# Kernel optimization log

Measured on AMD Instinct MI355X. Metric: run time of the kernel, lower is better.

The kernel has to match this reference:

```python
import jax, jax.numpy as jnp
import numpy as np

B, T, D, H = 2, 2048, 1024, 16
DK = D // H  # 64


def setup_inputs() -> dict:
    key = jax.random.key(0)
    ks = jax.random.split(key, 13)
    s = 1.0 / np.sqrt(D)
    return {
        "x": jax.random.normal(ks[0], (B, T, D), jnp.float32),
        "Wq_w": jax.random.normal(ks[1], (D, D), jnp.float32) * s,
        "Wq_b": jax.random.normal(ks[2], (D,), jnp.float32) * 0.01,
        "Wk_w": jax.random.normal(ks[3], (D, D), jnp.float32) * s,
        "Wk_b": jax.random.normal(ks[4], (D,), jnp.float32) * 0.01,
        "Wv_w": jax.random.normal(ks[5], (D, D), jnp.float32) * s,
        "Wv_b": jax.random.normal(ks[6], (D,), jnp.float32) * 0.01,
        "Wo_w": jax.random.normal(ks[7], (D, D), jnp.float32) * s,
        "Wo_b": jax.random.normal(ks[8], (D,), jnp.float32) * 0.01,
        "qr": jax.random.normal(ks[9], (B, H, T, DK), jnp.float32),
        "qi": jax.random.normal(ks[10], (B, H, T, DK), jnp.float32),
        "kr": jax.random.normal(ks[11], (B, H, T, DK), jnp.float32),
        "ki": jax.random.normal(ks[12], (B, H, T, DK), jnp.float32),
    }


def _heads(y):
    # [B,T,D] -> [B,H,T,DK]
    return y.reshape(B, T, H, DK).transpose(0, 2, 1, 3)


def reference(x, Wq_w, Wq_b, Wk_w, Wk_b, Wv_w, Wv_b, Wo_w, Wo_b, qr, qi, kr, ki):
    Q = _heads(x @ Wq_w.T + Wq_b)
    K = _heads(x @ Wk_w.T + Wk_b)
    V = _heads(x @ Wv_w.T + Wv_b)
    # quantum noise: sin(atan2(imag, real))
    Q = Q + jnp.sin(jnp.arctan2(qi, qr))
    K = K + jnp.sin(jnp.arctan2(ki, kr))
    # Recursive fractal attention collapses: branches are identical and
    # deterministic, so (A1+A2)/2 == depth-0 attention at every level.
    scores = jnp.einsum("bhtd,bhsd->bhts", Q, K) / np.sqrt(DK).astype(np.float32)
    weights = jax.nn.softmax(scores, axis=-1)
    attn = jnp.einsum("bhts,bhsd->bhtd", weights, V)  # [B,H,T,DK]
    out = attn.transpose(0, 2, 1, 3).reshape(B, T, D)
    return out @ Wo_w.T + Wo_b
```

## Files before the change

kernel.cpp:

```cpp
#include <hip/hip_runtime.h>
#include <hip/hip_fp16.h>
#include <stdint.h>

typedef _Float16 half_t;
typedef _Float16 hf2 __attribute__((ext_vector_type(2)));
typedef _Float16 hf4 __attribute__((ext_vector_type(4)));
typedef _Float16 hf8 __attribute__((ext_vector_type(8)));
typedef float f32x16 __attribute__((ext_vector_type(16)));
typedef unsigned uint2_t __attribute__((ext_vector_type(2)));

#define LOG2E 1.4426950408889634f

__device__ __forceinline__ void gload16(const void* g, void* l) {
  __builtin_amdgcn_global_load_lds(
      (const __attribute__((address_space(1))) unsigned int*)g,
      (__attribute__((address_space(3))) unsigned int*)l, 16, 0, 0);
}

__device__ __forceinline__ unsigned packrtz(float a, float b) {
  auto h = __builtin_amdgcn_cvt_pkrtz(a, b);
  union { decltype(h) h2; unsigned u; } c;
  c.h2 = h;
  return c.u;
}

__device__ __forceinline__ float exp2fast(float x) {
#if __has_builtin(__builtin_amdgcn_exp2f)
  return __builtin_amdgcn_exp2f(x);
#else
  return exp2f(x);
#endif
}

__device__ __forceinline__ float psum2(unsigned pw, hf2 ones, float acc) {
#if __has_builtin(__builtin_amdgcn_fdot2)
  union { unsigned u; hf2 h; } c;
  c.u = pw;
  return __builtin_amdgcn_fdot2(c.h, ones, acc, false);
#else
  union { unsigned u; hf2 h; } c;
  c.u = pw;
  return acc + (float)c.h[0] + (float)c.h[1];
#endif
}

__global__ __launch_bounds__(256) void cvt_kernel(
    const float* __restrict__ x, const float* __restrict__ wq,
    const float* __restrict__ wk, const float* __restrict__ wv,
    const float* __restrict__ wo, half_t* __restrict__ xh,
    half_t* __restrict__ wh) {
  long e = ((long)blockIdx.x * 256 + threadIdx.x) * 16;
  const float* src;
  half_t* dst;
  if (e < 4194304L) {
    src = x + e;
    dst = xh + e;
  } else {
    long j = e - 4194304L;
    int w = (int)(j >> 20);
    long off = j & 1048575L;
    src = (w == 0 ? wq : w == 1 ? wk : w == 2 ? wv : wo) + off;
    dst = wh + ((long)w << 20) + off;
  }
  const float4* s4 = (const float4*)src;
  float4 f0 = s4[0], f1 = s4[1], f2 = s4[2], f3 = s4[3];
  hf8 o0 = {(half_t)f0.x, (half_t)f0.y, (half_t)f0.z, (half_t)f0.w,
            (half_t)f1.x, (half_t)f1.y, (half_t)f1.z, (half_t)f1.w};
  hf8 o1 = {(half_t)f2.x, (half_t)f2.y, (half_t)f2.z, (half_t)f2.w,
            (half_t)f3.x, (half_t)f3.y, (half_t)f3.z, (half_t)f3.w};
  *(hf8*)dst = o0;
  *(hf8*)(dst + 8) = o1;
}

template <int CUR>
__device__ __forceinline__ void gstep(bool stage, const half_t* __restrict__ A,
                                      const half_t* __restrict__ Bt,
                                      char* ldsb, int wid, int& goA, int& goB,
                                      int aof0, int aof1, int aof2, int aof3,
                                      int bof0, int bof1, int bof2, int bof3,
                                      f32x16 acc[2][2]) {
  if (stage) {
#pragma unroll
    for (int i = 0; i < 4; i++) {
      gload16(A + goA + i * 32768,
              ldsb + (CUR ^ 1) * 16384 + i * 4096 + wid * 1024);
      gload16(Bt + goB + i * 32768,
              ldsb + 32768 + (CUR ^ 1) * 16384 + i * 4096 + wid * 1024);
    }
    goA += 64;
    goB += 64;
  }
#pragma unroll
  for (int kc = 0; kc < 4; kc++) {
    const int ao = (kc == 0 ? aof0 : kc == 1 ? aof1 : kc == 2 ? aof2 : aof3);
    const int bo = (kc == 0 ? bof0 : kc == 1 ? bof1 : kc == 2 ? bof2 : bof3);
    hf8 af0 = *(const hf8*)(ldsb + CUR * 16384 + ao);
    hf8 af1 = *(const hf8*)(ldsb + CUR * 16384 + ao + 4096);
    hf8 bf0 = *(const hf8*)(ldsb + 32768 + CUR * 16384 + bo);
    hf8 bf1 = *(const hf8*)(ldsb + 32768 + CUR * 16384 + bo + 4096);
    acc[0][0] =
        __builtin_amdgcn_mfma_f32_32x32x16_f16(af0, bf0, acc[0][0], 0, 0, 0);
    acc[0][1] =
        __builtin_amdgcn_mfma_f32_32x32x16_f16(af0, bf1, acc[0][1], 0, 0, 0);
    acc[1][0] =
        __builtin_amdgcn_mfma_f32_32x32x16_f16(af1, bf0, acc[1][0], 0, 0, 0);
    acc[1][1] =
        __builtin_amdgcn_mfma_f32_32x32x16_f16(af1, bf1, acc[1][1], 0, 0, 0);
  }
  __syncthreads();
}

__device__ __forceinline__ void gemm_core(const half_t* __restrict__ A,
                                          const half_t* __restrict__ Bt,
                                          int m0, int n0, char* ldsb,
                                          f32x16 acc[2][2]) {
  const int tid = threadIdx.x;
  const int wid = tid >> 6;
  const int lane = tid & 63;
  const int l31 = lane & 31;
  const int hh = lane >> 5;
  const int wm = wid >> 1, wn = wid & 1;

#pragma unroll
  for (int mt = 0; mt < 2; mt++)
#pragma unroll
    for (int nt = 0; nt < 2; nt++)
#pragma unroll
      for (int i = 0; i < 16; i++) acc[mt][nt][i] = 0.f;

  const int rowb = tid >> 3;
  const int c16 = (tid & 7) ^ (rowb & 7);
  int goA = (m0 + rowb) * 1024 + c16 * 8;
  int goB = (n0 + rowb) * 1024 + c16 * 8;

  const int swz0 = (hh * 16) ^ ((l31 & 7) << 4);
  const int swz1 = (32 + hh * 16) ^ ((l31 & 7) << 4);
  const int swz2 = (64 + hh * 16) ^ ((l31 & 7) << 4);
  const int swz3 = (96 + hh * 16) ^ ((l31 & 7) << 4);
  const int arow = (wm * 64 + l31) * 128;
  const int brow = (wn * 64 + l31) * 128;
  const int aof0 = arow + swz0, aof1 = arow + swz1, aof2 = arow + swz2,
            aof3 = arow + swz3;
  const int bof0 = brow + swz0, bof1 = brow + swz1, bof2 = brow + swz2,
            bof3 = brow + swz3;

#pragma unroll
  for (int i = 0; i < 4; i++) {
    gload16(A + goA + i * 32768, ldsb + i * 4096 + wid * 1024);
    gload16(Bt + goB + i * 32768, ldsb + 32768 + i * 4096 + wid * 1024);
  }
  goA += 64;
  goB += 64;
  __syncthreads();

  for (int kp = 0; kp < 8; ++kp) {
    gstep<0>(true, A, Bt, ldsb, wid, goA, goB, aof0, aof1, aof2, aof3, bof0,
             bof1, bof2, bof3, acc);
    gstep<1>(kp < 7, A, Bt, ldsb, wid, goA, goB, aof0, aof1, aof2, aof3, bof0,
             bof1, bof2, bof3, acc);
  }
}

__global__ __launch_bounds__(256, 2) void proj_kernel(
    const half_t* __restrict__ xh, const half_t* __restrict__ wh,
    const float* __restrict__ bq, const float* __restrict__ bk,
    const float* __restrict__ bv, const float* __restrict__ qr,
    const float* __restrict__ qi, const float* __restrict__ kr,
    const float* __restrict__ ki, half_t* __restrict__ Qh,
    half_t* __restrict__ Kh, half_t* __restrict__ Vth) {
  __shared__ __align__(16) char ldsb[65536];
  const int z = blockIdx.z;
  const half_t* Bt = wh + (size_t)z * 1048576;
  const int m0 = blockIdx.x * 128, n0 = blockIdx.y * 128;
  f32x16 acc[2][2];
  gemm_core(xh, Bt, m0, n0, ldsb, acc);

  const int tid = threadIdx.x;
  const int wid = tid >> 6;
  const int lane = tid & 63;
  const int l31 = lane & 31;
  const int hh = lane >> 5;
  const int wm = wid >> 1, wn = wid & 1;
  const float* bias = (z == 0) ? bq : (z == 1) ? bk : bv;
  const float* nr = (z == 0) ? qr : kr;
  const float* ni = (z == 0) ? qi : ki;
  const float scale = (z == 0) ? (0.125f * LOG2E) : 1.0f;

#pragma unroll
  for (int nt = 0; nt < 2; nt++) {
    const int n = n0 + wn * 64 + nt * 32 + l31;
    const float bsv = bias[n];
    const int hd = n >> 6, d = n & 63;
#pragma unroll
    for (int mt = 0; mt < 2; mt++) {
      const int mbase = m0 + wm * 64 + mt * 32;
      if (z == 2) {
#pragma unroll
        for (int g = 0; g < 4; g++) {
          const int m = mbase + 8 * g + 4 * hh;
          const int bb = m >> 11, tt = m & 2047;
          hf4 pk;
#pragma unroll
          for (int i2 = 0; i2 < 4; i2++)
            pk[i2] = (half_t)(acc[mt][nt][4 * g + i2] + bsv);
          *(hf4*)(Vth + (((size_t)(bb * 16 + hd) * 64 + d) * 2048 + tt)) = pk;
        }
      } else {
        half_t* dstp = (z == 0) ? Qh : Kh;
#pragma unroll
        for (int r = 0; r < 16; r++) {
          const int m = mbase + (r & 3) + 8 * (r >> 2) + 4 * hh;
          const int bb = m >> 11, tt = m & 2047;
          const size_t idx = ((size_t)(bb * 16 + hd) * 2048 + tt) * 64 + d;
          float v = acc[mt][nt][r] + bsv;
          const float a_ = nr[idx], b_ = ni[idx];
          v += b_ * rsqrtf(a_ * a_ + b_ * b_);
          dstp[idx] = (half_t)(v * scale);
        }
      }
    }
  }
}

template <int CUR>
__device__ __forceinline__ void attn_tile_t(
    bool stage, const half_t* __restrict__ Kb, const half_t* __restrict__ Vb,
    char* base, int qw, int& gk0, int& gk1, int& gv0, int& gv1,
    const int kofs[4], const hf8 qf[4], const f32x16& zv, f32x16 ot[2],
    float& psAcc, hf2 ones) {
  if (stage) {
    gload16(Kb + gk0, base + (CUR ^ 1) * 8192 + qw * 1024);
    gload16(Kb + gk1, base + (CUR ^ 1) * 8192 + 4096 + qw * 1024);
    gload16(Vb + gv0, base + 16384 + (CUR ^ 1) * 8192 + qw * 1024);
    gload16(Vb + gv1, base + 16384 + (CUR ^ 1) * 8192 + 4096 + qw * 1024);
    gk0 += 4096;
    gk1 += 4096;
    gv0 += 64;
    gv1 += 64;
  }
#pragma unroll
  for (int kt = 0; kt < 2; kt++) {
    __builtin_amdgcn_s_setprio(1);
    f32x16 s = __builtin_amdgcn_mfma_f32_32x32x16_f16(
        *(const hf8*)(base + kofs[0] + CUR * 8192 + kt * 4096), qf[0], zv, 0, 0,
        0);
    s = __builtin_amdgcn_mfma_f32_32x32x16_f16(
        *(const hf8*)(base + kofs[1] + CUR * 8192 + kt * 4096), qf[1], s, 0, 0,
        0);
    s = __builtin_amdgcn_mfma_f32_32x32x16_f16(
        *(const hf8*)(base + kofs[2] + CUR * 8192 + kt * 4096), qf[2], s, 0, 0,
        0);
    s = __builtin_amdgcn_mfma_f32_32x32x16_f16(
        *(const hf8*)(base + kofs[3] + CUR * 8192 + kt * 4096), qf[3], s, 0, 0,
        0);
    __builtin_amdgcn_s_setprio(0);

    unsigned pw[8];
#pragma unroll
    for (int j = 0; j < 8; j++) {
      float p0 = exp2fast(s[2 * j]);
      float p1 = exp2fast(s[2 * j + 1]);
      pw[j] = packrtz(p0, p1);
      psAcc = psum2(pw[j], ones, psAcc);
    }

#pragma unroll
    for (int sub = 0; sub < 2; sub++) {
      const int kc = kt * 2 + sub;
      unsigned a0 = pw[sub * 4 + 0], a1 = pw[sub * 4 + 1];
      unsigned a2 = pw[sub * 4 + 2], a3 = pw[sub * 4 + 3];
      union { unsigned u[4]; hf8 v; } pu;
#if __has_builtin(__builtin_amdgcn_permlane32_swap)
      uint2_t r02 = __builtin_amdgcn_permlane32_swap(a0, a2, false, false);
      uint2_t r13 = __builtin_amdgcn_permlane32_swap(a1, a3, false, false);
      pu.u[0] = r02[0];
      pu.u[1] = r13[0];
      pu.u[2] = r02[1];
      pu.u[3] = r13[1];
#else
      const int hh_ = (threadIdx.x & 63) >> 5;
      unsigned x0 = __shfl_xor(a0, 32, 64), x1 = __shfl_xor(a1, 32, 64);
      unsigned x2 = __shfl_xor(a2, 32, 64), x3 = __shfl_xor(a3, 32, 64);
      pu.u[0] = hh_ ? x2 : a0;
      pu.u[1] = hh_ ? x3 : a1;
      pu.u[2] = hh_ ? a2 : x0;
      pu.u[3] = hh_ ? a3 : x1;
#endif
      __builtin_amdgcn_s_setprio(1);
#pragma unroll
      for (int dt = 0; dt < 2; dt++) {
        hf8 vf =
            *(const hf8*)(base + kofs[kc] + 16384 + CUR * 8192 + dt * 4096);
        ot[dt] =
            __builtin_amdgcn_mfma_f32_32x32x16_f16(vf, pu.v, ot[dt], 0, 0, 0);
      }
      __builtin_amdgcn_s_setprio(0);
    }
  }
  __syncthreads();
}

__global__ __launch_bounds__(512, 4) void attn_kernel(
    const half_t* __restrict__ Qh, const half_t* __restrict__ Kh,
    const half_t* __restrict__ Vth, half_t* __restrict__ ah) {
  __shared__ __align__(16) char smem[65536];
  const int tid = threadIdx.x, wid = tid >> 6, lane = tid & 63;
  const int l31 = lane & 31, hh = lane >> 5;
  const int qw = wid & 3, g = wid >> 2;
  const int lin = blockIdx.x;
  const int slot = lin >> 3;
  const int bh = (lin & 7) * 4 + (slot >> 4);
  const int qb = slot & 15;
  const int b = bh >> 4, hd = bh & 15;
  const int t = qb * 128 + qw * 32 + l31;

  char* base = smem + g * 32768;

  const half_t* qrow = Qh + ((size_t)bh * 2048 + t) * 64;
  hf8 qf[4];
#pragma unroll
  for (int kc = 0; kc < 4; kc++) qf[kc] = *(const hf8*)(qrow + kc * 16 + hh * 8);

  f32x16 ot[2];
#pragma unroll
  for (int dt = 0; dt < 2; dt++)
#pragma unroll
    for (int i = 0; i < 16; i++) ot[dt][i] = 0.f;
  f32x16 zv;
#pragma unroll
  for (int i = 0; i < 16; i++) zv[i] = 0.f;
  float psAcc = 0.f;
  const hf2 ones = {(_Float16)1.0f, (_Float16)1.0f};

  const half_t* Kb = Kh + (size_t)bh * 2048 * 64;
  const half_t* Vb = Vth + (size_t)bh * 64 * 2048;
  const int kvbase = g * 1024;

  int kofs[4];
#pragma unroll
  for (int kc = 0; kc < 4; kc++)
    kofs[kc] = l31 * 128 + ((kc * 32 + hh * 16) ^ ((l31 & 7) << 4));

  int gk0, gk1, gv0, gv1;
  {
    int c0 = qw * 64 + lane, c1 = 256 + qw * 64 + lane;
    int r0 = c0 >> 3, s0 = (c0 & 7) ^ (r0 & 7);
    int r1 = c1 >> 3, s1 = (c1 & 7) ^ (r1 & 7);
    gk0 = (kvbase + r0) * 64 + s0 * 8;
    gk1 = (kvbase + r1) * 64 + s1 * 8;
    gv0 = r0 * 2048 + kvbase + s0 * 8;
    gv1 = r1 * 2048 + kvbase + s1 * 8;
  }
  gload16(Kb + gk0, base + qw * 1024);
  gload16(Kb + gk1, base + 4096 + qw * 1024);
  gload16(Vb + gv0, base + 16384 + qw * 1024);
  gload16(Vb + gv1, base + 16384 + 4096 + qw * 1024);
  gk0 += 4096;
  gk1 += 4096;
  gv0 += 64;
  gv1 += 64;
  __syncthreads();

  for (int tp = 0; tp < 8; ++tp) {
    attn_tile_t<0>(true, Kb, Vb, base, qw, gk0, gk1, gv0, gv1, kofs, qf, zv,
                   ot, psAcc, ones);
    attn_tile_t<1>(tp < 7, Kb, Vb, base, qw, gk0, gk1, gv0, gv1, kofs, qf, zv,
                   ot, psAcc, ones);
  }

  const float lrun = psAcc + __shfl_xor(psAcc, 32, 64);

  float* cb = (float*)smem;
  float* lb = (float*)(smem + 32768);
  if (g == 1) {
#pragma unroll
    for (int dt = 0; dt < 2; dt++)
#pragma unroll
      for (int i = 0; i < 16; i++)
        cb[((qw * 2 + dt) * 16 + i) * 64 + lane] = ot[dt][i];
    lb[qw * 64 + lane] = lrun;
  }
  __syncthreads();
  if (g == 0) {
#pragma unroll
    for (int dt = 0; dt < 2; dt++)
#pragma unroll
      for (int i = 0; i < 16; i++)
        ot[dt][i] += cb[((qw * 2 + dt) * 16 + i) * 64 + lane];
    const float inv = 1.0f / (lrun + lb[qw * 64 + lane]);
    const size_t obase = ((size_t)b * 2048 + t) * 1024 + hd * 64;
#pragma unroll
    for (int dt = 0; dt < 2; dt++)
#pragma unroll
      for (int gg = 0; gg < 4; gg++) {
        hf4 pk;
#pragma unroll
        for (int i2 = 0; i2 < 4; i2++)
          pk[i2] = (half_t)(ot[dt][4 * gg + i2] * inv);
        *(hf4*)(ah + obase + dt * 32 + 8 * gg + 4 * hh) = pk;
      }
  }
}

__global__ __launch_bounds__(256, 2) void outproj_kernel(
    const half_t* __restrict__ ah, const half_t* __restrict__ woh,
    const float* __restrict__ bo, float* __restrict__ out) {
  __shared__ __align__(16) char ldsb[65536];
  const int m0 = blockIdx.x * 128, n0 = blockIdx.y * 128;
  f32x16 acc[2][2];
  gemm_core(ah, woh, m0, n0, ldsb, acc);
  const int tid = threadIdx.x, wid = tid >> 6, lane = tid & 63;
  const int l31 = lane & 31, hh = lane >> 5;
  const int wm = wid >> 1, wn = wid & 1;
#pragma unroll
  for (int nt = 0; nt < 2; nt++) {
    const int n = n0 + wn * 64 + nt * 32 + l31;
    const float bsv = bo[n];
#pragma unroll
    for (int mt = 0; mt < 2; mt++) {
      const int mbase = m0 + wm * 64 + mt * 32;
#pragma unroll
      for (int r = 0; r < 16; r++) {
        const int m = mbase + (r & 3) + 8 * (r >> 2) + 4 * hh;
        out[(size_t)m * 1024 + n] = acc[mt][nt][r] + bsv;
      }
    }
  }
}

extern "C" void kernel_launch(void* const* d_in, const int* in_sizes, int n_in,
                              void* d_out, int out_size, void* d_ws,
                              size_t ws_size, hipStream_t stream) {
  const float* x = (const float*)d_in[0];
  const float* Wq = (const float*)d_in[1];
  const float* bq = (const float*)d_in[2];
  const float* Wk = (const float*)d_in[3];
  const float* bk = (const float*)d_in[4];
  const float* Wv = (const float*)d_in[5];
  const float* bv = (const float*)d_in[6];
  const float* Wo = (const float*)d_in[7];
  const float* bo = (const float*)d_in[8];
  const float* qr = (const float*)d_in[9];
  const float* qi = (const float*)d_in[10];
  const float* kr = (const float*)d_in[11];
  const float* ki = (const float*)d_in[12];
  float* out = (float*)d_out;

  char* ws = (char*)d_ws;
  half_t* xh = (half_t*)(ws);
  half_t* wh = (half_t*)(ws + 8388608);
  half_t* Qh = (half_t*)(ws + 16777216);
  half_t* Kh = (half_t*)(ws + 25165824);
  half_t* Vth = (half_t*)(ws + 33554432);
  half_t* ah = (half_t*)(ws + 41943040);

  cvt_kernel<<<dim3(2048), dim3(256), 0, stream>>>(x, Wq, Wk, Wv, Wo, xh, wh);
  proj_kernel<<<dim3(32, 8, 3), dim3(256), 0, stream>>>(
      xh, wh, bq, bk, bv, qr, qi, kr, ki, Qh, Kh, Vth);
  attn_kernel<<<dim3(512), dim3(512), 0, stream>>>(Qh, Kh, Vth, ah);
  outproj_kernel<<<dim3(32, 8), dim3(256), 0, stream>>>(ah, wh + 3 * 1048576, bo,
                                                        out);
}
```

Measured before the change: 110.8 us.

## Shrink GEMM tiles to 128x64 and drop LDS double buffering for occupancy

The projection and output-projection GEMMs move from 128x128 tiles with double-buffered LDS (64KB) to 128x64 tiles with a single 24KB LDS buffer. Each wave now holds two accumulators instead of four. Grids double along N and launch bounds rise to 4 blocks per SM, trading software pipelining and per-tile data reuse for more resident waves and more blocks. Loads are no longer overlapped with MFMA inside a block, and the A tile is re-read twice as often across blocks.

```diff
diff --git a/kernel.cpp b/kernel.cpp
--- a/kernel.cpp
+++ b/kernel.cpp
@@ -72,48 +72,10 @@
   *(hf8*)(dst + 8) = o1;
 }
 
-template <int CUR>
-__device__ __forceinline__ void gstep(bool stage, const half_t* __restrict__ A,
-                                      const half_t* __restrict__ Bt,
-                                      char* ldsb, int wid, int& goA, int& goB,
-                                      int aof0, int aof1, int aof2, int aof3,
-                                      int bof0, int bof1, int bof2, int bof3,
-                                      f32x16 acc[2][2]) {
-  if (stage) {
-#pragma unroll
-    for (int i = 0; i < 4; i++) {
-      gload16(A + goA + i * 32768,
-              ldsb + (CUR ^ 1) * 16384 + i * 4096 + wid * 1024);
-      gload16(Bt + goB + i * 32768,
-              ldsb + 32768 + (CUR ^ 1) * 16384 + i * 4096 + wid * 1024);
-    }
-    goA += 64;
-    goB += 64;
-  }
-#pragma unroll
-  for (int kc = 0; kc < 4; kc++) {
-    const int ao = (kc == 0 ? aof0 : kc == 1 ? aof1 : kc == 2 ? aof2 : aof3);
-    const int bo = (kc == 0 ? bof0 : kc == 1 ? bof1 : kc == 2 ? bof2 : bof3);
-    hf8 af0 = *(const hf8*)(ldsb + CUR * 16384 + ao);
-    hf8 af1 = *(const hf8*)(ldsb + CUR * 16384 + ao + 4096);
-    hf8 bf0 = *(const hf8*)(ldsb + 32768 + CUR * 16384 + bo);
-    hf8 bf1 = *(const hf8*)(ldsb + 32768 + CUR * 16384 + bo + 4096);
-    acc[0][0] =
-        __builtin_amdgcn_mfma_f32_32x32x16_f16(af0, bf0, acc[0][0], 0, 0, 0);
-    acc[0][1] =
-        __builtin_amdgcn_mfma_f32_32x32x16_f16(af0, bf1, acc[0][1], 0, 0, 0);
-    acc[1][0] =
-        __builtin_amdgcn_mfma_f32_32x32x16_f16(af1, bf0, acc[1][0], 0, 0, 0);
-    acc[1][1] =
-        __builtin_amdgcn_mfma_f32_32x32x16_f16(af1, bf1, acc[1][1], 0, 0, 0);
-  }
-  __syncthreads();
-}
-
 __device__ __forceinline__ void gemm_core(const half_t* __restrict__ A,
                                           const half_t* __restrict__ Bt,
                                           int m0, int n0, char* ldsb,
-                                          f32x16 acc[2][2]) {
+                                          f32x16 acc[2]) {
   const int tid = threadIdx.x;
   const int wid = tid >> 6;
   const int lane = tid & 63;
@@ -124,9 +86,7 @@
 #pragma unroll
   for (int mt = 0; mt < 2; mt++)
 #pragma unroll
-    for (int nt = 0; nt < 2; nt++)
-#pragma unroll
-      for (int i = 0; i < 16; i++) acc[mt][nt][i] = 0.f;
+    for (int i = 0; i < 16; i++) acc[mt][i] = 0.f;
 
   const int rowb = tid >> 3;
   const int c16 = (tid & 7) ^ (rowb & 7);
@@ -138,41 +98,48 @@
   const int swz2 = (64 + hh * 16) ^ ((l31 & 7) << 4);
   const int swz3 = (96 + hh * 16) ^ ((l31 & 7) << 4);
   const int arow = (wm * 64 + l31) * 128;
-  const int brow = (wn * 64 + l31) * 128;
+  const int brow = 16384 + (wn * 32 + l31) * 128;
   const int aof0 = arow + swz0, aof1 = arow + swz1, aof2 = arow + swz2,
             aof3 = arow + swz3;
   const int bof0 = brow + swz0, bof1 = brow + swz1, bof2 = brow + swz2,
             bof3 = brow + swz3;
 
-#pragma unroll
-  for (int i = 0; i < 4; i++) {
-    gload16(A + goA + i * 32768, ldsb + i * 4096 + wid * 1024);
-    gload16(Bt + goB + i * 32768, ldsb + 32768 + i * 4096 + wid * 1024);
-  }
-  goA += 64;
-  goB += 64;
-  __syncthreads();
-
-  for (int kp = 0; kp < 8; ++kp) {
-    gstep<0>(true, A, Bt, ldsb, wid, goA, goB, aof0, aof1, aof2, aof3, bof0,
-             bof1, bof2, bof3, acc);
-    gstep<1>(kp < 7, A, Bt, ldsb, wid, goA, goB, aof0, aof1, aof2, aof3, bof0,
-             bof1, bof2, bof3, acc);
-  }
-}
-
-__global__ __launch_bounds__(256, 2) void proj_kernel(
+  for (int kt = 0; kt < 16; ++kt) {
+#pragma unroll
+    for (int i = 0; i < 4; i++)
+      gload16(A + goA + i * 32768, ldsb + i * 4096 + wid * 1024);
+#pragma unroll
+    for (int i = 0; i < 2; i++)
+      gload16(Bt + goB + i * 32768, ldsb + 16384 + i * 4096 + wid * 1024);
+    goA += 64;
+    goB += 64;
+    __syncthreads();
+#pragma unroll
+    for (int kc = 0; kc < 4; kc++) {
+      const int ao = (kc == 0 ? aof0 : kc == 1 ? aof1 : kc == 2 ? aof2 : aof3);
+      const int bo = (kc == 0 ? bof0 : kc == 1 ? bof1 : kc == 2 ? bof2 : bof3);
+      hf8 af0 = *(const hf8*)(ldsb + ao);
+      hf8 af1 = *(const hf8*)(ldsb + ao + 4096);
+      hf8 bf = *(const hf8*)(ldsb + bo);
+      acc[0] = __builtin_amdgcn_mfma_f32_32x32x16_f16(af0, bf, acc[0], 0, 0, 0);
+      acc[1] = __builtin_amdgcn_mfma_f32_32x32x16_f16(af1, bf, acc[1], 0, 0, 0);
+    }
+    __syncthreads();
+  }
+}
+
+__global__ __launch_bounds__(256, 4) void proj_kernel(
     const half_t* __restrict__ xh, const half_t* __restrict__ wh,
     const float* __restrict__ bq, const float* __restrict__ bk,
     const float* __restrict__ bv, const float* __restrict__ qr,
     const float* __restrict__ qi, const float* __restrict__ kr,
     const float* __restrict__ ki, half_t* __restrict__ Qh,
     half_t* __restrict__ Kh, half_t* __restrict__ Vth) {
-  __shared__ __align__(16) char ldsb[65536];
+  __shared__ __align__(16) char ldsb[24576];
   const int z = blockIdx.z;
   const half_t* Bt = wh + (size_t)z * 1048576;
-  const int m0 = blockIdx.x * 128, n0 = blockIdx.y * 128;
-  f32x16 acc[2][2];
+  const int m0 = blockIdx.x * 128, n0 = blockIdx.y * 64;
+  f32x16 acc[2];
   gemm_core(xh, Bt, m0, n0, ldsb, acc);
 
   const int tid = threadIdx.x;
@@ -186,37 +153,34 @@
   const float* ni = (z == 0) ? qi : ki;
   const float scale = (z == 0) ? (0.125f * LOG2E) : 1.0f;
 
-#pragma unroll
-  for (int nt = 0; nt < 2; nt++) {
-    const int n = n0 + wn * 64 + nt * 32 + l31;
-    const float bsv = bias[n];
-    const int hd = n >> 6, d = n & 63;
-#pragma unroll
-    for (int mt = 0; mt < 2; mt++) {
-      const int mbase = m0 + wm * 64 + mt * 32;
-      if (z == 2) {
-#pragma unroll
-        for (int g = 0; g < 4; g++) {
-          const int m = mbase + 8 * g + 4 * hh;
-          const int bb = m >> 11, tt = m & 2047;
-          hf4 pk;
-#pragma unroll
-          for (int i2 = 0; i2 < 4; i2++)
-            pk[i2] = (half_t)(acc[mt][nt][4 * g + i2] + bsv);
-          *(hf4*)(Vth + (((size_t)(bb * 16 + hd) * 64 + d) * 2048 + tt)) = pk;
-        }
-      } else {
-        half_t* dstp = (z == 0) ? Qh : Kh;
-#pragma unroll
-        for (int r = 0; r < 16; r++) {
-          const int m = mbase + (r & 3) + 8 * (r >> 2) + 4 * hh;
-          const int bb = m >> 11, tt = m & 2047;
-          const size_t idx = ((size_t)(bb * 16 + hd) * 2048 + tt) * 64 + d;
-          float v = acc[mt][nt][r] + bsv;
-          const float a_ = nr[idx], b_ = ni[idx];
-          v += b_ * rsqrtf(a_ * a_ + b_ * b_);
-          dstp[idx] = (half_t)(v * scale);
-        }
+  const int n = n0 + wn * 32 + l31;
+  const float bsv = bias[n];
+  const int hd = n >> 6, d = n & 63;
+#pragma unroll
+  for (int mt = 0; mt < 2; mt++) {
+    const int mbase = m0 + wm * 64 + mt * 32;
+    if (z == 2) {
+#pragma unroll
+      for (int g = 0; g < 4; g++) {
+        const int m = mbase + 8 * g + 4 * hh;
+        const int bb = m >> 11, tt = m & 2047;
+        hf4 pk;
+#pragma unroll
+        for (int i2 = 0; i2 < 4; i2++)
+          pk[i2] = (half_t)(acc[mt][4 * g + i2] + bsv);
+        *(hf4*)(Vth + (((size_t)(bb * 16 + hd) * 64 + d) * 2048 + tt)) = pk;
+      }
+    } else {
+      half_t* dstp = (z == 0) ? Qh : Kh;
+#pragma unroll
+      for (int r = 0; r < 16; r++) {
+        const int m = mbase + (r & 3) + 8 * (r >> 2) + 4 * hh;
+        const int bb = m >> 11, tt = m & 2047;
+        const size_t idx = ((size_t)(bb * 16 + hd) * 2048 + tt) * 64 + d;
+        float v = acc[mt][r] + bsv;
+        const float a_ = nr[idx], b_ = ni[idx];
+        v += b_ * rsqrtf(a_ * a_ + b_ * b_);
+        dstp[idx] = (half_t)(v * scale);
       }
     }
   }
@@ -402,28 +366,25 @@
   }
 }
 
-__global__ __launch_bounds__(256, 2) void outproj_kernel(
+__global__ __launch_bounds__(256, 4) void outproj_kernel(
     const half_t* __restrict__ ah, const half_t* __restrict__ woh,
     const float* __restrict__ bo, float* __restrict__ out) {
-  __shared__ __align__(16) char ldsb[65536];
-  const int m0 = blockIdx.x * 128, n0 = blockIdx.y * 128;
-  f32x16 acc[2][2];
+  __shared__ __align__(16) char ldsb[24576];
+  const int m0 = blockIdx.x * 128, n0 = blockIdx.y * 64;
+  f32x16 acc[2];
   gemm_core(ah, woh, m0, n0, ldsb, acc);
   const int tid = threadIdx.x, wid = tid >> 6, lane = tid & 63;
   const int l31 = lane & 31, hh = lane >> 5;
   const int wm = wid >> 1, wn = wid & 1;
-#pragma unroll
-  for (int nt = 0; nt < 2; nt++) {
-    const int n = n0 + wn * 64 + nt * 32 + l31;
-    const float bsv = bo[n];
-#pragma unroll
-    for (int mt = 0; mt < 2; mt++) {
-      const int mbase = m0 + wm * 64 + mt * 32;
-#pragma unroll
-      for (int r = 0; r < 16; r++) {
-        const int m = mbase + (r & 3) + 8 * (r >> 2) + 4 * hh;
-        out[(size_t)m * 1024 + n] = acc[mt][nt][r] + bsv;
-      }
+  const int n = n0 + wn * 32 + l31;
+  const float bsv = bo[n];
+#pragma unroll
+  for (int mt = 0; mt < 2; mt++) {
+    const int mbase = m0 + wm * 64 + mt * 32;
+#pragma unroll
+    for (int r = 0; r < 16; r++) {
+      const int m = mbase + (r & 3) + 8 * (r >> 2) + 4 * hh;
+      out[(size_t)m * 1024 + n] = acc[mt][r] + bsv;
     }
   }
 }
@@ -455,9 +416,9 @@
   half_t* ah = (half_t*)(ws + 41943040);
 
   cvt_kernel<<<dim3(2048), dim3(256), 0, stream>>>(x, Wq, Wk, Wv, Wo, xh, wh);
-  proj_kernel<<<dim3(32, 8, 3), dim3(256), 0, stream>>>(
+  proj_kernel<<<dim3(32, 16, 3), dim3(256), 0, stream>>>(
       xh, wh, bq, bk, bv, qr, qi, kr, ki, Qh, Kh, Vth);
   attn_kernel<<<dim3(512), dim3(512), 0, stream>>>(Qh, Kh, Vth, ah);
-  outproj_kernel<<<dim3(32, 8), dim3(256), 0, stream>>>(ah, wh + 3 * 1048576, bo,
-                                                        out);
-}
+  outproj_kernel<<<dim3(32, 16), dim3(256), 0, stream>>>(ah, wh + 3 * 1048576,
+                                                         bo, out);
+}
```

Result: slower. 113.5 us (+2.4%).
